# Optimization experiments

Hardware: AMD Instinct MI355X
Metric: run time of the kernel (lower is better)

## Reference

```python
import jax, jax.numpy as jnp
import numpy as np

B = 256        # trees per batch
DEPTH = 10     # complete binary tree depth -> 2^10 - 1 = 1023 internal nodes
N = 2**DEPTH - 1
IN = 128       # input_size
H = 128        # hidden_size
C = 5          # num_classes


def setup_inputs() -> dict:
    key = jax.random.key(0)
    ks = jax.random.split(key, 13)
    gdim = IN + 2 * H  # concat(x, h_left, h_right)
    inp = {"x": jax.random.normal(ks[0], (B, N, IN), jnp.float32)}
    names = ["i", "fl", "fr", "o", "u"]
    for j, nm in enumerate(names):
        inp[f"W_{nm}"] = 0.05 * jax.random.normal(ks[1 + 2 * j], (H, gdim), jnp.float32)
        inp[f"b_{nm}"] = 0.05 * jax.random.normal(ks[2 + 2 * j], (H,), jnp.float32)
    inp["W_cls"] = 0.05 * jax.random.normal(ks[11], (C, H), jnp.float32)
    inp["b_cls"] = 0.05 * jax.random.normal(ks[12], (C,), jnp.float32)
    return inp


def reference(x, W_i, b_i, W_fl, b_fl, W_fr, b_fr, W_o, b_o, W_u, b_u, W_cls, b_cls):
    # Level-order complete binary tree: node k has children 2k+1, 2k+2.
    # Bottom-up sweep; below the deepest internal level all children are
    # empty nodes with h = c = 0 (matches the original base case).
    Bb = x.shape[0]
    h = jnp.zeros((Bb, 2 ** DEPTH, H), x.dtype)
    c = jnp.zeros_like(h)
    for d in range(DEPTH - 1, -1, -1):  # fixed, small structural loop
        n = 2 ** d
        start = n - 1  # level-order offset of level d
        xs = x[:, start:start + n]            # [B, n, IN]
        hl, hr = h[:, 0::2], h[:, 1::2]       # children of node j are 2j, 2j+1 (level-local)
        cl, cr = c[:, 0::2], c[:, 1::2]
        comb = jnp.concatenate([xs, hl, hr], axis=-1)  # [B, n, IN+2H]
        lin = lambda W, b: jnp.einsum('bng,og->bno', comb, W) + b
        i = jax.nn.sigmoid(lin(W_i, b_i))
        fl = jax.nn.sigmoid(lin(W_fl, b_fl))
        fr = jax.nn.sigmoid(lin(W_fr, b_fr))
        o = jax.nn.sigmoid(lin(W_o, b_o))
        u = jnp.tanh(lin(W_u, b_u))
        c = i * u + fl * cl + fr * cr
        h = o * jnp.tanh(c)
    root_h = h[:, 0]                          # [B, H]
    logits = root_h @ W_cls.T + b_cls         # [B, C]
    return logits
```

## Files before the change

kernel.cpp:

```cpp
#include <hip/hip_runtime.h>
#include <hip/hip_bf16.h>
#include <stdint.h>


#define BATCH 256
#define NTOT 1023
#define HDIM 128
#define NCLS 5
#define GDIM 384
#define NBLKC 128

typedef __bf16 bf16x8 __attribute__((ext_vector_type(8)));
typedef float f32x4 __attribute__((ext_vector_type(4)));

__device__ unsigned g_ctr;
__device__ unsigned g_base;

__device__ __forceinline__ float sigmoid_f(float v) { return 1.f / (1.f + __expf(-v)); }
__device__ __forceinline__ float tanh_f(float v) { return 1.f - 2.f / (1.f + __expf(2.f * v)); }

__device__ __forceinline__ void load_lds16(const void* g, void* l) {
  __builtin_amdgcn_global_load_lds((const __attribute__((address_space(1))) unsigned int*)g,
                                   (__attribute__((address_space(3))) unsigned int*)l, 16, 0, 0);
}

__device__ __forceinline__ void gbar(unsigned base, unsigned k) {
  __syncthreads();
  if (threadIdx.x == 0) {
    __threadfence();
    __hip_atomic_fetch_add(&g_ctr, 1u, __ATOMIC_RELAXED, __HIP_MEMORY_SCOPE_AGENT);
    while ((unsigned)(__hip_atomic_load(&g_ctr, __ATOMIC_RELAXED, __HIP_MEMORY_SCOPE_AGENT) - base)
           < k * (unsigned)NBLKC)
      __builtin_amdgcn_s_sleep(1);
    (void)__hip_atomic_load(&g_ctr, __ATOMIC_ACQUIRE, __HIP_MEMORY_SCOPE_AGENT);
  }
  __syncthreads();
}

__global__ __launch_bounds__(256) void pack_w(
    const float* __restrict__ W0, const float* __restrict__ W1, const float* __restrict__ W2,
    const float* __restrict__ W3, const float* __restrict__ W4, __bf16* __restrict__ PW)
{
  int t = blockIdx.x * 256 + threadIdx.x;
  int lane = t & 63;
  int chunk = t >> 6;
  int ks = chunk % 12;
  int jf = (chunk / 12) & 7;
  int g = chunk / 96;
  const float* W = (g == 0) ? W0 : (g == 1) ? W1 : (g == 2) ? W2 : (g == 3) ? W3 : W4;
  const float* s = W + (size_t)(jf * 16 + (lane & 15)) * GDIM + ks * 32 + (lane >> 4) * 8;
  float4 v0 = *(const float4*)s;
  float4 v1 = *(const float4*)(s + 4);
  bf16x8 w;
  w[0] = (__bf16)v0.x; w[1] = (__bf16)v0.y; w[2] = (__bf16)v0.z; w[3] = (__bf16)v0.w;
  w[4] = (__bf16)v1.x; w[5] = (__bf16)v1.y; w[6] = (__bf16)v1.z; w[7] = (__bf16)v1.w;
  *(bf16x8*)(PW + (size_t)t * 8) = w;
}

template<bool LEAF>
__device__ __forceinline__ void tile_body(
    const float* __restrict__ x, const __bf16* __restrict__ PW,
    const __bf16* __restrict__ h_prev, const float* __restrict__ c_prev,
    __bf16* __restrict__ h_out, float* __restrict__ c_out,
    const float* __restrict__ bv0, const float* __restrict__ bv1,
    const float* __restrict__ bv2, const float* __restrict__ bv3,
    const float* __restrict__ bv4,
    int d, int m0, int j0, unsigned char* lds)
{
  const int tid = threadIdx.x;
  const int w = tid >> 6;
  const int l = tid & 63;
  const int l15 = l & 15;
  const int quad = l >> 4;
  const int q8 = quad * 8;
  const int mh = w & 1, jh = w >> 1;
  const int n = 1 << d;
  const int jfb = j0 >> 4;
  constexpr int NKT = LEAF ? 4 : 12;
  constexpr int NBC = LEAF ? 3 : 5;

  const int ms = m0 + w * 16 + l15;
  const int bs = ms >> d;
  const int ids = ms & (n - 1);
  const float* xrow = x + ((size_t)bs * NTOT + (n - 1) + ids) * HDIM;
  const __bf16* hrow = LEAF ? (const __bf16*)nullptr
                            : h_prev + ((size_t)bs * 2 * n + 2 * ids) * HDIM;

  auto stage = [&](int ks) {
    unsigned char* Ab = lds + (ks & 1) * 24576;
    unsigned char* Bb = Ab + 4096;
#pragma unroll
    for (int q = 0; q < NBC; ++q) {
      int c = w * NBC + q;
      int g;
      if (LEAF) { const int gm[3] = {0, 3, 4}; g = gm[c >> 2]; }
      else g = c >> 2;
      int jfl = c & 3;
      const __bf16* s = PW + (((size_t)(g * 8 + jfb + jfl) * 12 + ks) * 64 + l) * 8;
      load_lds16(s, Bb + (g * 4 + jfl) * 1024);
    }
    if (LEAF || ks < 4) {
      const float* s = xrow + ks * 32 + q8;
      float4 v0 = *(const float4*)s;
      float4 v1 = *(const float4*)(s + 4);
      bf16x8 wv;
      wv[0] = (__bf16)v0.x; wv[1] = (__bf16)v0.y; wv[2] = (__bf16)v0.z; wv[3] = (__bf16)v0.w;
      wv[4] = (__bf16)v1.x; wv[5] = (__bf16)v1.y; wv[6] = (__bf16)v1.z; wv[7] = (__bf16)v1.w;
      *(bf16x8*)(Ab + w * 1024 + l * 16) = wv;
    } else {
      int off = (ks < 8) ? (ks - 4) * 32 : 128 + (ks - 8) * 32;
      load_lds16(hrow + off + q8, Ab + w * 1024);
    }
  };

  f32x4 acc[2][2][5];
#pragma unroll
  for (int mf = 0; mf < 2; ++mf)
#pragma unroll
    for (int jfl = 0; jfl < 2; ++jfl)
#pragma unroll
      for (int g = 0; g < 5; ++g)
        acc[mf][jfl][g] = (f32x4){0.f, 0.f, 0.f, 0.f};

  stage(0);
  for (int ks = 0; ks < NKT; ++ks) {
    __syncthreads();
    if (ks + 1 < NKT) stage(ks + 1);
    const unsigned char* Ab = lds + (ks & 1) * 24576;
    const unsigned char* Bb = Ab + 4096;
    bf16x8 a0 = *(const bf16x8*)(Ab + (mh * 2 + 0) * 1024 + l * 16);
    bf16x8 a1 = *(const bf16x8*)(Ab + (mh * 2 + 1) * 1024 + l * 16);
#pragma unroll
    for (int g = 0; g < 5; ++g) {
      if (LEAF && (g == 1 || g == 2)) continue;
#pragma unroll
      for (int jfl = 0; jfl < 2; ++jfl) {
        bf16x8 bb = *(const bf16x8*)(Bb + (g * 4 + jh * 2 + jfl) * 1024 + l * 16);
        acc[0][jfl][g] = __builtin_amdgcn_mfma_f32_16x16x32_bf16(a0, bb, acc[0][jfl][g], 0, 0, 0);
        acc[1][jfl][g] = __builtin_amdgcn_mfma_f32_16x16x32_bf16(a1, bb, acc[1][jfl][g], 0, 0, 0);
      }
    }
  }

#pragma unroll
  for (int jfl = 0; jfl < 2; ++jfl) {
    const int je = j0 + jh * 32 + jfl * 16 + l15;
    const float b0 = bv0[je], b1 = bv1[je], b2 = bv2[je], b3 = bv3[je], b4 = bv4[je];
#pragma unroll
    for (int mf = 0; mf < 2; ++mf) {
#pragma unroll
      for (int r = 0; r < 4; ++r) {
        int me = m0 + mh * 32 + mf * 16 + quad * 4 + r;
        int b = me >> d;
        int id = me & (n - 1);
        float gi = sigmoid_f(acc[mf][jfl][0][r] + b0);
        float go = sigmoid_f(acc[mf][jfl][3][r] + b3);
        float gu = tanh_f(acc[mf][jfl][4][r] + b4);
        float cv = gi * gu;
        if (!LEAF) {
          float gl = sigmoid_f(acc[mf][jfl][1][r] + b1);
          float gr = sigmoid_f(acc[mf][jfl][2][r] + b2);
          size_t cbase = ((size_t)b * 2 * n + 2 * id) * HDIM + je;
          cv += gl * c_prev[cbase] + gr * c_prev[cbase + HDIM];
        }
        size_t ob = ((size_t)b * n + id) * HDIM + je;
        c_out[ob] = cv;
        h_out[ob] = (__bf16)(go * tanh_f(cv));
      }
    }
  }
}

template<bool LEAF>
__global__ __launch_bounds__(256, 2) void level_kernel(
    const float* __restrict__ x, const __bf16* __restrict__ PW,
    const float* __restrict__ bv0, const float* __restrict__ bv1,
    const float* __restrict__ bv2, const float* __restrict__ bv3,
    const float* __restrict__ bv4,
    const __bf16* __restrict__ h_prev, const float* __restrict__ c_prev,
    __bf16* __restrict__ h_out, float* __restrict__ c_out, int d)
{
  __shared__ unsigned char lds[49152];
  tile_body<LEAF>(x, PW, h_prev, c_prev, h_out, c_out,
                  bv0, bv1, bv2, bv3, bv4, d,
                  (int)blockIdx.x * 64, (int)blockIdx.y * 64, lds);
}

__global__ __launch_bounds__(256, 2) void tail_kernel(
    const float* __restrict__ x, const __bf16* __restrict__ PW,
    const float* __restrict__ bv0, const float* __restrict__ bv1,
    const float* __restrict__ bv2, const float* __restrict__ bv3,
    const float* __restrict__ bv4,
    const float* __restrict__ Wcls, const float* __restrict__ bcls,
    __bf16* hb0, __bf16* hb1, float* cb0, float* cb1, float* out)
{
  __shared__ unsigned char lds[49152];
  const unsigned base = g_base;
  unsigned k = 1;
  for (int d = 5; d >= 0; --d, ++k) {
    const int p = 9 - d;
    __bf16* h_out = (p & 1) ? hb1 : hb0;
    float*  c_out = (p & 1) ? cb1 : cb0;
    const __bf16* h_prev = (p & 1) ? hb0 : hb1;
    const float*  c_prev = (p & 1) ? cb0 : cb1;
    const int units = ((BATCH << d) >> 6) * 2;
    for (int u = blockIdx.x; u < units; u += NBLKC) {
      tile_body<false>(x, PW, h_prev, c_prev, h_out, c_out,
                       bv0, bv1, bv2, bv3, bv4, d,
                       (u >> 1) * 64, (u & 1) * 64, lds);
    }
    gbar(base, k);
  }
  if (blockIdx.x == 0) {
    if (threadIdx.x < BATCH) {
      const __bf16* hr = hb1 + (size_t)threadIdx.x * HDIM;
      float s[NCLS];
#pragma unroll
      for (int c = 0; c < NCLS; ++c) s[c] = bcls[c];
      for (int kk = 0; kk < HDIM; ++kk) {
        float hv = (float)hr[kk];
#pragma unroll
        for (int c = 0; c < NCLS; ++c) s[c] += hv * Wcls[c * HDIM + kk];
      }
#pragma unroll
      for (int c = 0; c < NCLS; ++c) out[threadIdx.x * NCLS + c] = s[c];
    }
    if (threadIdx.x == 0)
      __hip_atomic_store(&g_base, base + 6u * (unsigned)NBLKC,
                         __ATOMIC_RELAXED, __HIP_MEMORY_SCOPE_AGENT);
  }
}

extern "C" void kernel_launch(void* const* d_in, const int* in_sizes, int n_in,
                              void* d_out, int out_size, void* d_ws, size_t ws_size,
                              hipStream_t stream) {
  const float* x  = (const float*)d_in[0];
  const float* W[5]  = {(const float*)d_in[1], (const float*)d_in[3], (const float*)d_in[5],
                        (const float*)d_in[7], (const float*)d_in[9]};
  const float* bv[5] = {(const float*)d_in[2], (const float*)d_in[4], (const float*)d_in[6],
                        (const float*)d_in[8], (const float*)d_in[10]};
  const float* Wcls = (const float*)d_in[11];
  const float* bcls = (const float*)d_in[12];

  uint8_t* ws = (uint8_t*)d_ws;
  __bf16* hb0 = (__bf16*)ws;
  __bf16* hb1 = (__bf16*)(ws + 33554432);
  float*  cb0 = (float*)(ws + 50331648);
  float*  cb1 = (float*)(ws + 117440512);
  __bf16* PW  = (__bf16*)(ws + 150994944);

  pack_w<<<120, 256, 0, stream>>>(W[0], W[1], W[2], W[3], W[4], PW);

  level_kernel<true><<<dim3(2048, 2), 256, 0, stream>>>(
      x, PW, bv[0], bv[1], bv[2], bv[3], bv[4], hb1, cb1, hb0, cb0, 9);
  for (int d = 8; d >= 6; --d) {
    const int p = 9 - d;
    __bf16* h_out = (p & 1) ? hb1 : hb0;
    float*  c_out = (p & 1) ? cb1 : cb0;
    const __bf16* h_prev = (p & 1) ? hb0 : hb1;
    const float*  c_prev = (p & 1) ? cb0 : cb1;
    dim3 grid((BATCH << d) >> 6, 2);
    level_kernel<false><<<grid, 256, 0, stream>>>(
        x, PW, bv[0], bv[1], bv[2], bv[3], bv[4], h_prev, c_prev, h_out, c_out, d);
  }
  tail_kernel<<<NBLKC, 256, 0, stream>>>(
      x, PW, bv[0], bv[1], bv[2], bv[3], bv[4],
      Wcls, bcls, hb0, hb1, cb0, cb1, (float*)d_out);
}
```

Measured before the change: 542.5 us.

## Replace grid-barrier tail with per-tree LDS-resident subtree kernel

The tail levels 5..0 previously ran on 128 persistent blocks that synchronised through a global atomic barrier, with h/c going through global memory. Now each of 256 blocks owns one tree's top 63-node subtree. It keeps h and c in ping-pong LDS buffers (swizzled h, padded c), streams the weights through double-buffered LDS, and computes the classifier per block. This removes the grid barriers and the global round trips, at the cost of a large LDS footprint (one block per CU) and wasted MFMA work on the small upper levels.

```diff
diff --git a/kernel.cpp b/kernel.cpp
--- a/kernel.cpp
+++ b/kernel.cpp
@@ -8,13 +8,9 @@
 #define HDIM 128
 #define NCLS 5
 #define GDIM 384
-#define NBLKC 128
 
 typedef __bf16 bf16x8 __attribute__((ext_vector_type(8)));
 typedef float f32x4 __attribute__((ext_vector_type(4)));
-
-__device__ unsigned g_ctr;
-__device__ unsigned g_base;
 
 __device__ __forceinline__ float sigmoid_f(float v) { return 1.f / (1.f + __expf(-v)); }
 __device__ __forceinline__ float tanh_f(float v) { return 1.f - 2.f / (1.f + __expf(2.f * v)); }
@@ -22,19 +18,6 @@
 __device__ __forceinline__ void load_lds16(const void* g, void* l) {
   __builtin_amdgcn_global_load_lds((const __attribute__((address_space(1))) unsigned int*)g,
                                    (__attribute__((address_space(3))) unsigned int*)l, 16, 0, 0);
-}
-
-__device__ __forceinline__ void gbar(unsigned base, unsigned k) {
-  __syncthreads();
-  if (threadIdx.x == 0) {
-    __threadfence();
-    __hip_atomic_fetch_add(&g_ctr, 1u, __ATOMIC_RELAXED, __HIP_MEMORY_SCOPE_AGENT);
-    while ((unsigned)(__hip_atomic_load(&g_ctr, __ATOMIC_RELAXED, __HIP_MEMORY_SCOPE_AGENT) - base)
-           < k * (unsigned)NBLKC)
-      __builtin_amdgcn_s_sleep(1);
-    (void)__hip_atomic_load(&g_ctr, __ATOMIC_ACQUIRE, __HIP_MEMORY_SCOPE_AGENT);
-  }
-  __syncthreads();
 }
 
 __global__ __launch_bounds__(256) void pack_w(
@@ -186,48 +169,156 @@
                   (int)blockIdx.x * 64, (int)blockIdx.y * 64, lds);
 }
 
-__global__ __launch_bounds__(256, 2) void tail_kernel(
+#define TB_P  81920
+#define TB_Q  132096
+#define CSTR  132
+
+__global__ __launch_bounds__(256, 1) void tail_kernel(
     const float* __restrict__ x, const __bf16* __restrict__ PW,
     const float* __restrict__ bv0, const float* __restrict__ bv1,
     const float* __restrict__ bv2, const float* __restrict__ bv3,
     const float* __restrict__ bv4,
     const float* __restrict__ Wcls, const float* __restrict__ bcls,
-    __bf16* hb0, __bf16* hb1, float* cb0, float* cb1, float* out)
+    const __bf16* __restrict__ h6, const float* __restrict__ c6,
+    float* __restrict__ out)
 {
-  __shared__ unsigned char lds[49152];
-  const unsigned base = g_base;
-  unsigned k = 1;
-  for (int d = 5; d >= 0; --d, ++k) {
-    const int p = 9 - d;
-    __bf16* h_out = (p & 1) ? hb1 : hb0;
-    float*  c_out = (p & 1) ? cb1 : cb0;
-    const __bf16* h_prev = (p & 1) ? hb0 : hb1;
-    const float*  c_prev = (p & 1) ? cb0 : cb1;
-    const int units = ((BATCH << d) >> 6) * 2;
-    for (int u = blockIdx.x; u < units; u += NBLKC) {
-      tile_body<false>(x, PW, h_prev, c_prev, h_out, c_out,
-                       bv0, bv1, bv2, bv3, bv4, d,
-                       (u >> 1) * 64, (u & 1) * 64, lds);
-    }
-    gbar(base, k);
-  }
-  if (blockIdx.x == 0) {
-    if (threadIdx.x < BATCH) {
-      const __bf16* hr = hb1 + (size_t)threadIdx.x * HDIM;
-      float s[NCLS];
-#pragma unroll
-      for (int c = 0; c < NCLS; ++c) s[c] = bcls[c];
-      for (int kk = 0; kk < HDIM; ++kk) {
-        float hv = (float)hr[kk];
-#pragma unroll
-        for (int c = 0; c < NCLS; ++c) s[c] += hv * Wcls[c * HDIM + kk];
-      }
-#pragma unroll
-      for (int c = 0; c < NCLS; ++c) out[threadIdx.x * NCLS + c] = s[c];
-    }
-    if (threadIdx.x == 0)
-      __hip_atomic_store(&g_base, base + 6u * (unsigned)NBLKC,
-                         __ATOMIC_RELAXED, __HIP_MEMORY_SCOPE_AGENT);
+  __shared__ unsigned char lds[157184];
+  const int b = blockIdx.x;
+  const int tid = threadIdx.x;
+  const int w = tid >> 6;
+  const int l = tid & 63;
+  const int l15 = l & 15;
+  const int quad = l >> 4;
+  const int q8 = quad * 8;
+
+  unsigned char* Ph = lds + TB_P;
+  float* Pc = (float*)(lds + TB_P + 16384);
+  unsigned char* Qh = lds + TB_Q;
+  float* Qc = (float*)(lds + TB_Q + 8192);
+
+  {
+    const __bf16* hs = h6 + (size_t)b * 64 * HDIM;
+#pragma unroll
+    for (int it = 0; it < 4; ++it) {
+      int idx = it * 256 + tid;
+      int node = idx >> 4, i8 = idx & 15;
+      bf16x8 v = *(const bf16x8*)(hs + node * HDIM + i8 * 8);
+      *(bf16x8*)(Ph + node * 256 + ((i8 * 16) ^ ((node & 7) << 4))) = v;
+    }
+    const float* cs = c6 + (size_t)b * 64 * HDIM;
+#pragma unroll
+    for (int it = 0; it < 8; ++it) {
+      int idx = it * 256 + tid;
+      int node = idx >> 5, seg = idx & 31;
+      float4 v = *(const float4*)(cs + node * HDIM + seg * 4);
+      *(float4*)(Pc + node * CSTR + seg * 4) = v;
+    }
+  }
+
+  for (int d = 5; d >= 0; --d) {
+    const int s = 5 - d;
+    const int n = 1 << d;
+    const int nmf = (d == 5) ? 2 : 1;
+    unsigned char* prev_h = (s & 1) ? Qh : Ph;
+    float*         prev_c = (s & 1) ? Qc : Pc;
+    unsigned char* cur_h  = (s & 1) ? Ph : Qh;
+    float*         cur_c  = (s & 1) ? Pc : Qc;
+
+    bf16x8 xf[2][4];
+#pragma unroll
+    for (int mf = 0; mf < 2; ++mf) {
+      const float* xr = x + ((size_t)b * NTOT + (n - 1) + mf * 16 + l15) * HDIM + q8;
+#pragma unroll
+      for (int ks = 0; ks < 4; ++ks) {
+        float4 v0 = *(const float4*)(xr + ks * 32);
+        float4 v1 = *(const float4*)(xr + ks * 32 + 4);
+        bf16x8 t;
+        t[0] = (__bf16)v0.x; t[1] = (__bf16)v0.y; t[2] = (__bf16)v0.z; t[3] = (__bf16)v0.w;
+        t[4] = (__bf16)v1.x; t[5] = (__bf16)v1.y; t[6] = (__bf16)v1.z; t[7] = (__bf16)v1.w;
+        xf[mf][ks] = t;
+      }
+    }
+
+    auto stageB = [&](int ks) {
+      unsigned char* Bb = lds + (ks & 1) * 40960;
+#pragma unroll
+      for (int q = 0; q < 10; ++q) {
+        int c = w * 10 + q;
+        const __bf16* src = PW + ((size_t)(c * 12 + ks) * 64 + l) * 8;
+        load_lds16(src, Bb + c * 1024);
+      }
+    };
+
+    f32x4 acc[2][2][5];
+#pragma unroll
+    for (int mf = 0; mf < 2; ++mf)
+#pragma unroll
+      for (int jfl = 0; jfl < 2; ++jfl)
+#pragma unroll
+        for (int g = 0; g < 5; ++g)
+          acc[mf][jfl][g] = (f32x4){0.f, 0.f, 0.f, 0.f};
+
+    stageB(0);
+    for (int ks = 0; ks < 12; ++ks) {
+      __syncthreads();
+      if (ks < 11) stageB(ks + 1);
+      const unsigned char* Bb = lds + (ks & 1) * 40960;
+      bf16x8 a0, a1;
+      if (ks < 4) {
+        a0 = xf[0][ks];
+        a1 = xf[1][ks];
+      } else {
+        const int o = (ks < 8) ? 0 : 1;
+        const int col2 = (((ks - (o ? 8 : 4)) * 32) + q8) * 2;
+        int n0 = 2 * l15 + o;
+        int n1 = 2 * (16 + l15) + o;
+        a0 = *(const bf16x8*)(prev_h + n0 * 256 + (col2 ^ ((n0 & 7) << 4)));
+        a1 = *(const bf16x8*)(prev_h + n1 * 256 + (col2 ^ ((n1 & 7) << 4)));
+      }
+#pragma unroll
+      for (int g = 0; g < 5; ++g) {
+#pragma unroll
+        for (int jfl = 0; jfl < 2; ++jfl) {
+          bf16x8 bb = *(const bf16x8*)(Bb + (g * 8 + w * 2 + jfl) * 1024 + l * 16);
+          acc[0][jfl][g] = __builtin_amdgcn_mfma_f32_16x16x32_bf16(a0, bb, acc[0][jfl][g], 0, 0, 0);
+          if (nmf == 2)
+            acc[1][jfl][g] = __builtin_amdgcn_mfma_f32_16x16x32_bf16(a1, bb, acc[1][jfl][g], 0, 0, 0);
+        }
+      }
+    }
+
+#pragma unroll
+    for (int jfl = 0; jfl < 2; ++jfl) {
+      const int je = w * 32 + jfl * 16 + l15;
+      const float b0 = bv0[je], b1 = bv1[je], b2 = bv2[je], b3 = bv3[je], b4 = bv4[je];
+#pragma unroll
+      for (int mf = 0; mf < 2; ++mf) {
+#pragma unroll
+        for (int r = 0; r < 4; ++r) {
+          const int me = mf * 16 + quad * 4 + r;
+          if (me < n) {
+            float gi = sigmoid_f(acc[mf][jfl][0][r] + b0);
+            float gl = sigmoid_f(acc[mf][jfl][1][r] + b1);
+            float gr = sigmoid_f(acc[mf][jfl][2][r] + b2);
+            float go = sigmoid_f(acc[mf][jfl][3][r] + b3);
+            float gu = tanh_f(acc[mf][jfl][4][r] + b4);
+            float cv = gi * gu + gl * prev_c[(2 * me) * CSTR + je]
+                               + gr * prev_c[(2 * me + 1) * CSTR + je];
+            cur_c[me * CSTR + je] = cv;
+            *(__bf16*)(cur_h + me * 256 + ((je * 2) ^ ((me & 7) << 4))) =
+                (__bf16)(go * tanh_f(cv));
+          }
+        }
+      }
+    }
+  }
+
+  __syncthreads();
+  if (tid < NCLS) {
+    float sacc = bcls[tid];
+    for (int k = 0; k < HDIM; ++k)
+      sacc += (float)(*(const __bf16*)(Ph + k * 2)) * Wcls[tid * HDIM + k];
+    out[(size_t)b * NCLS + tid] = sacc;
   }
 }
 
@@ -263,7 +354,7 @@
     level_kernel<false><<<grid, 256, 0, stream>>>(
         x, PW, bv[0], bv[1], bv[2], bv[3], bv[4], h_prev, c_prev, h_out, c_out, d);
   }
-  tail_kernel<<<NBLKC, 256, 0, stream>>>(
+  tail_kernel<<<BATCH, 256, 0, stream>>>(
       x, PW, bv[0], bv[1], bv[2], bv[3], bv[4],
-      Wcls, bcls, hb0, hb1, cb0, cb1, (float*)d_out);
-}
+      Wcls, bcls, hb1, cb1, (float*)d_out);
+}
```

Result: faster. 457.3 us (-15.7%).
